# Performance work log

Measured on AMD Instinct MI355X. Metric: run time of the kernel, lower is better.

The kernel has to match this reference:

```python
import jax, jax.numpy as jnp
import numpy as np

SIZE = 4096


def fast_hadamard_transform(x, normalize=True):
    """Walsh-Hadamard transform along last dim via log2(n) butterfly stages."""
    orig_shape = x.shape
    n = orig_shape[-1]
    h = 1
    while h < n:
        # view as (..., n//(2h), 2, h) and butterfly the pair axis
        x = x.reshape(orig_shape[:-1] + (n // (2 * h), 2, h))
        a = x[..., 0, :]
        b = x[..., 1, :]
        x = jnp.stack([a + b, a - b], axis=-2).reshape(orig_shape)
        h *= 2
    if normalize:
        x = x * (1.0 / np.sqrt(n)).astype(x.dtype)
    return x


def setup_inputs() -> dict:
    key = jax.random.key(0)
    kx, ks, kb = jax.random.split(key, 3)
    x = jax.random.normal(kx, (4, 4096, SIZE), dtype=jnp.float32)
    # adaptive_init: scale ~ N(1.0, 0.1), shift ~ N(0.0, 0.01)
    scale = 1.0 + 0.1 * jax.random.normal(ks, (SIZE,), dtype=jnp.float32)
    shift = 0.01 * jax.random.normal(kb, (SIZE,), dtype=jnp.float32)
    return {"x": x, "scale": scale, "shift": shift}


def reference(x, scale, shift):
    x_h = fast_hadamard_transform(x, normalize=True)
    return scale * x_h + shift
```

## Files before the change

kernel.cpp:

```cpp
#include <hip/hip_runtime.h>


#define ROW 4096
#define STR 17

typedef int intx1;

__device__ __forceinline__ void wht16(float v[16]) {
#pragma unroll
  for (int h = 1; h < 16; h <<= 1) {
#pragma unroll
    for (int i = 0; i < 16; ++i) {
      if ((i & h) == 0) {
        float a = v[i], b = v[i | h];
        v[i] = a + b;
        v[i | h] = a - b;
      }
    }
  }
}

template <int PAT>
__device__ __forceinline__ void swz_step(float v[16], float sgn) {
#pragma unroll
  for (int j = 0; j < 16; ++j) {
    const int pi = __builtin_amdgcn_ds_swizzle(__float_as_int(v[j]), PAT);
    v[j] = fmaf(sgn, v[j], __int_as_float(pi));
  }
}

__global__ __launch_bounds__(256, 8) void AdaptiveHadamardTransform_kernel(
    const float* __restrict__ x, const float* __restrict__ scale,
    const float* __restrict__ shift, float* __restrict__ out) {
  __shared__ float lds[256 * STR];

  const int t = threadIdx.x;
  const int lane = t & 63;
  const long long base = (long long)blockIdx.x * ROW;

  float v[16];

  {
    const float4* __restrict__ x4 =
        reinterpret_cast<const float4*>(x + base + 16 * t);
#pragma unroll
    for (int q = 0; q < 4; ++q) {
      const float4 f = x4[q];
      v[4 * q + 0] = f.x;
      v[4 * q + 1] = f.y;
      v[4 * q + 2] = f.z;
      v[4 * q + 3] = f.w;
    }
  }

  wht16(v);

  swz_step<0x041F>(v, (lane & 1) ? -1.f : 1.f);
  swz_step<0x081F>(v, (lane & 2) ? -1.f : 1.f);
  swz_step<0x101F>(v, (lane & 4) ? -1.f : 1.f);
  swz_step<0x201F>(v, (lane & 8) ? -1.f : 1.f);

#pragma unroll
  for (int j = 0; j < 16; ++j) lds[t * STR + j] = v[j];
  __syncthreads();
  {
    const int i1 = t >> 4, i0 = t & 15;
#pragma unroll
    for (int r = 0; r < 16; ++r) v[r] = lds[(r * 16 + i1) * STR + i0];
  }

  wht16(v);

  const float norm = 0.015625f;
#pragma unroll
  for (int r = 0; r < 16; ++r) {
    const int c = r * 256 + t;
    const float o = fmaf(scale[c], v[r] * norm, shift[c]);
    __builtin_nontemporal_store(o, out + base + c);
  }
}

extern "C" void kernel_launch(void* const* d_in, const int* in_sizes, int n_in,
                              void* d_out, int out_size, void* d_ws, size_t ws_size,
                              hipStream_t stream) {
  const float* x = (const float*)d_in[0];
  const float* scale = (const float*)d_in[1];
  const float* shift = (const float*)d_in[2];
  float* out = (float*)d_out;

  const int rows = in_sizes[0] / ROW;
  AdaptiveHadamardTransform_kernel<<<rows, 256, 0, stream>>>(x, scale, shift, out);
}
```

Baseline: 437.2 us.

## Process two rows per block to overlap row computation and amortize loads

```diff
diff --git a/kernel.cpp b/kernel.cpp
--- a/kernel.cpp
+++ b/kernel.cpp
@@ -3,8 +3,6 @@
 
 #define ROW 4096
 #define STR 17
-
-typedef int intx1;
 
 __device__ __forceinline__ void wht16(float v[16]) {
 #pragma unroll
@@ -29,6 +27,13 @@
   }
 }
 
+__device__ __forceinline__ void swz_mid(float v[16], int lane) {
+  swz_step<0x041F>(v, (lane & 1) ? -1.f : 1.f);
+  swz_step<0x081F>(v, (lane & 2) ? -1.f : 1.f);
+  swz_step<0x101F>(v, (lane & 4) ? -1.f : 1.f);
+  swz_step<0x201F>(v, (lane & 8) ? -1.f : 1.f);
+}
+
 __global__ __launch_bounds__(256, 8) void AdaptiveHadamardTransform_kernel(
     const float* __restrict__ x, const float* __restrict__ scale,
     const float* __restrict__ shift, float* __restrict__ out) {
@@ -36,47 +41,71 @@
 
   const int t = threadIdx.x;
   const int lane = t & 63;
-  const long long base = (long long)blockIdx.x * ROW;
+  const long long baseA = (long long)blockIdx.x * (2 * ROW);
+  const long long baseB = baseA + ROW;
 
-  float v[16];
+  float a[16], b[16];
 
   {
-    const float4* __restrict__ x4 =
-        reinterpret_cast<const float4*>(x + base + 16 * t);
+    const float4* __restrict__ a4 =
+        reinterpret_cast<const float4*>(x + baseA + 16 * t);
+    const float4* __restrict__ b4 =
+        reinterpret_cast<const float4*>(x + baseB + 16 * t);
 #pragma unroll
     for (int q = 0; q < 4; ++q) {
-      const float4 f = x4[q];
-      v[4 * q + 0] = f.x;
-      v[4 * q + 1] = f.y;
-      v[4 * q + 2] = f.z;
-      v[4 * q + 3] = f.w;
+      const float4 f = a4[q];
+      a[4 * q + 0] = f.x;
+      a[4 * q + 1] = f.y;
+      a[4 * q + 2] = f.z;
+      a[4 * q + 3] = f.w;
+    }
+#pragma unroll
+    for (int q = 0; q < 4; ++q) {
+      const float4 f = b4[q];
+      b[4 * q + 0] = f.x;
+      b[4 * q + 1] = f.y;
+      b[4 * q + 2] = f.z;
+      b[4 * q + 3] = f.w;
     }
   }
 
-  wht16(v);
+  const float norm = 0.015625f;
+  const int i1 = t >> 4, i0 = t & 15;
 
-  swz_step<0x041F>(v, (lane & 1) ? -1.f : 1.f);
-  swz_step<0x081F>(v, (lane & 2) ? -1.f : 1.f);
-  swz_step<0x101F>(v, (lane & 4) ? -1.f : 1.f);
-  swz_step<0x201F>(v, (lane & 8) ? -1.f : 1.f);
+  wht16(a);
+  swz_mid(a, lane);
+#pragma unroll
+  for (int j = 0; j < 16; ++j) lds[t * STR + j] = a[j];
+
+  wht16(b);
+  swz_mid(b, lane);
+
+  __syncthreads();
 
 #pragma unroll
-  for (int j = 0; j < 16; ++j) lds[t * STR + j] = v[j];
-  __syncthreads();
-  {
-    const int i1 = t >> 4, i0 = t & 15;
-#pragma unroll
-    for (int r = 0; r < 16; ++r) v[r] = lds[(r * 16 + i1) * STR + i0];
-  }
-
-  wht16(v);
-
-  const float norm = 0.015625f;
+  for (int r = 0; r < 16; ++r) a[r] = lds[(r * 16 + i1) * STR + i0];
+  wht16(a);
 #pragma unroll
   for (int r = 0; r < 16; ++r) {
     const int c = r * 256 + t;
-    const float o = fmaf(scale[c], v[r] * norm, shift[c]);
-    __builtin_nontemporal_store(o, out + base + c);
+    const float o = fmaf(scale[c], a[r] * norm, shift[c]);
+    __builtin_nontemporal_store(o, out + baseA + c);
+  }
+
+  __syncthreads();
+
+#pragma unroll
+  for (int j = 0; j < 16; ++j) lds[t * STR + j] = b[j];
+  __syncthreads();
+
+#pragma unroll
+  for (int r = 0; r < 16; ++r) b[r] = lds[(r * 16 + i1) * STR + i0];
+  wht16(b);
+#pragma unroll
+  for (int r = 0; r < 16; ++r) {
+    const int c = r * 256 + t;
+    const float o = fmaf(scale[c], b[r] * norm, shift[c]);
+    __builtin_nontemporal_store(o, out + baseB + c);
   }
 }
 
@@ -89,5 +118,5 @@
   float* out = (float*)d_out;
 
   const int rows = in_sizes[0] / ROW;
-  AdaptiveHadamardTransform_kernel<<<rows, 256, 0, stream>>>(x, scale, shift, out);
+  AdaptiveHadamardTransform_kernel<<<rows / 2, 256, 0, stream>>>(x, scale, shift, out);
 }
```

Result: slower. 457.2 us (+4.6%).
